# Optimization experiments

Measured on AMD Instinct MI355X. Metric: run time of the kernel, lower is better.

Reference implementation:

```python
import jax, jax.numpy as jnp
import numpy as np


def _gcn_conv(X, src, dst, norm, W, n_nodes):
    # gather + normalized aggregate (SpMM) then dense linear (GEMM)
    msg = X[src] * norm[:, None]                       # [E, F]
    agg = jax.ops.segment_sum(msg, dst, num_segments=n_nodes)  # [N, F]
    return agg @ W                                     # [N, F_out]


def setup_inputs() -> dict:
    key = jax.random.key(0)
    k1, k2, k3, k4, k5 = jax.random.split(key, 5)
    N, E, D_IN, D_HID, D_OUT = 50000, 800000, 128, 128, 64
    X = jax.random.normal(k1, (N, D_IN), dtype=jnp.float32)
    edge_index = jax.random.randint(k2, (2, E), 0, N, dtype=jnp.int64)
    s = 1.0 / np.sqrt(D_IN)
    W1 = jax.random.normal(k3, (D_IN, D_HID), dtype=jnp.float32) * s
    W2 = jax.random.normal(k4, (D_HID, D_HID), dtype=jnp.float32) * s
    W3 = jax.random.normal(k5, (D_HID, D_OUT), dtype=jnp.float32) * s
    return {"X": X, "edge_index": edge_index, "W1": W1, "W2": W2, "W3": W3}


def reference(X, edge_index, W1, W2, W3):
    n_nodes = X.shape[0]
    src, dst = edge_index[0], edge_index[1]
    # symmetric degree normalization D^-1/2 A D^-1/2 (degrees from edge list)
    ones = jnp.ones(src.shape[0], dtype=X.dtype)
    deg = jax.ops.segment_sum(ones, dst, num_segments=n_nodes)
    deg = jnp.maximum(deg, 1.0)
    dinv = jax.lax.rsqrt(deg)
    norm = dinv[src] * dinv[dst]                       # [E]
    h = jax.nn.relu(_gcn_conv(X, src, dst, norm, W1, n_nodes))
    h = jax.nn.relu(_gcn_conv(h, src, dst, norm, W2, n_nodes))
    h = jax.nn.relu(_gcn_conv(h, src, dst, norm, W3, n_nodes))
    return jax.nn.softmax(h, axis=-1)
```

## Files before the change

### kernel.cpp

```cpp
#include <hip/hip_runtime.h>
#include <hip/hip_bf16.h>

typedef __attribute__((ext_vector_type(8))) short short8;
typedef __attribute__((ext_vector_type(4))) short short4v;
typedef __attribute__((ext_vector_type(4))) float f32x4;

static inline size_t ws_align(size_t x) { return (x + 511) & ~((size_t)511); }

static __device__ inline unsigned short f2bf(float f) {
    __hip_bfloat16 h = __float2bfloat16(f);
    return __builtin_bit_cast(unsigned short, h);
}

static __device__ inline float bf2f(unsigned short u) {
    unsigned int x = ((unsigned int)u) << 16;
    return __builtin_bit_cast(float, x);
}

__global__ void sniff_kernel(const unsigned short* __restrict__ w1,
                             const unsigned int* __restrict__ ei,
                             int* __restrict__ flags) {
    int i = threadIdx.x;
    unsigned e = (w1[2 * i] >> 7) & 0xFF;
    unsigned long long m1 = __ballot(e >= 100 && e <= 130);
    unsigned long long m2 = __ballot(ei[2 * i + 1] == 0u);
    if (i == 0) {
        flags[0] = (__popcll(m1) < 48) ? 1 : 0;
        flags[1] = (__popcll(m2) >= 48) ? 1 : 0;
    }
}

__global__ void hist_kernel(const int* __restrict__ ei, const int* __restrict__ flags,
                            int* __restrict__ counts, int* __restrict__ loff, int E) {
    int e = blockIdx.x * blockDim.x + threadIdx.x;
    if (e < E) {
        int d = flags[1] ? ei[2 * (size_t)E + 2 * e] : ei[(size_t)E + e];
        loff[e] = atomicAdd(&counts[d], 1);
    }
}

__global__ __launch_bounds__(256) void alloc_kernel(const int* __restrict__ counts,
                                                    float* __restrict__ dinv,
                                                    int* __restrict__ rowptr,
                                                    int* __restrict__ total, int N) {
    int n = blockIdx.x * blockDim.x + threadIdx.x;
    int lane = threadIdx.x & 63;
    int c = (n < N) ? counts[n] : 0;
    if (n < N) {
        int d = (c < 1) ? 1 : c;
        dinv[n] = rsqrtf((float)d);
    }
    int incl = c;
#pragma unroll
    for (int off = 1; off < 64; off <<= 1) {
        int v = __shfl_up(incl, off, 64);
        if (lane >= off) incl += v;
    }
    int wavetot = __shfl(incl, 63, 64);
    int base = 0;
    if (lane == 0) base = atomicAdd(total, wavetot);
    base = __shfl(base, 0, 64);
    if (n < N) rowptr[n] = base + incl - c;
}

__global__ void fill_kernel(const int* __restrict__ ei, const int* __restrict__ flags,
                            const float* __restrict__ dinv, const int* __restrict__ rowptr,
                            const int* __restrict__ loff, int2* __restrict__ edgedat, int E) {
    int e = blockIdx.x * blockDim.x + threadIdx.x;
    if (e < E) {
        int s, d;
        if (flags[1]) {
            s = ei[2 * e];
            d = ei[2 * (size_t)E + 2 * e];
        } else {
            s = ei[e];
            d = ei[(size_t)E + e];
        }
        int pos = rowptr[d] + loff[e];
        float wt = dinv[s] * dinv[d];
        edgedat[pos] = make_int2(s, __float_as_int(wt));
    }
}


template <int FOUT>
__global__ __launch_bounds__(256) void gemm_kernel(const void* __restrict__ Araw, int a_follows,
                                                   const void* __restrict__ Wraw,
                                                   const int* __restrict__ flags,
                                                   unsigned short* __restrict__ out, int Nrows) {
    constexpr int K = 128;
    constexpr int NT = FOUT / 16;
    constexpr int LDB = K + 8;
    __shared__ __align__(16) unsigned short bt[FOUT * LDB];

    const int tid = threadIdx.x;
    const int in_fp32 = flags[0];
    const int a_fp32 = a_follows & in_fp32;

    constexpr int TOT4 = K * FOUT / 4;
    if (in_fp32) {
        const float* Wf = (const float*)Wraw;
        for (int i = tid; i < TOT4; i += 256) {
            int idx = i * 4;
            int k = idx / FOUT;
            int n = idx & (FOUT - 1);
            float4 v = *(const float4*)(const void*)(Wf + idx);
            bt[(n + 0) * LDB + k] = f2bf(v.x);
            bt[(n + 1) * LDB + k] = f2bf(v.y);
            bt[(n + 2) * LDB + k] = f2bf(v.z);
            bt[(n + 3) * LDB + k] = f2bf(v.w);
        }
    } else {
        const unsigned short* Ws = (const unsigned short*)Wraw;
        for (int i = tid; i < TOT4; i += 256) {
            int idx = i * 4;
            int k = idx / FOUT;
            int n = idx & (FOUT - 1);
            short4v v = *(const short4v*)(const void*)(Ws + idx);
#pragma unroll
            for (int j = 0; j < 4; j++) bt[(n + j) * LDB + k] = ((const unsigned short*)&v)[j];
        }
    }

    const int wave = tid >> 6;
    const int lane = tid & 63;
    const int quad = lane >> 4;
    const int r16 = lane & 15;

    short8 afrag[2][4];
#pragma unroll
    for (int t = 0; t < 2; t++) {
        int arow = blockIdx.x * 128 + t * 64 + wave * 16 + r16;
        if (arow > Nrows - 1) arow = Nrows - 1;
        if (a_fp32) {
            const float* Ap = (const float*)Araw + (size_t)arow * K + quad * 8;
#pragma unroll
            for (int kk = 0; kk < 4; kk++) {
                float4 f0 = *(const float4*)(const void*)(Ap + kk * 32);
                float4 f1 = *(const float4*)(const void*)(Ap + kk * 32 + 4);
                short8 r;
                r[0] = (short)f2bf(f0.x); r[1] = (short)f2bf(f0.y);
                r[2] = (short)f2bf(f0.z); r[3] = (short)f2bf(f0.w);
                r[4] = (short)f2bf(f1.x); r[5] = (short)f2bf(f1.y);
                r[6] = (short)f2bf(f1.z); r[7] = (short)f2bf(f1.w);
                afrag[t][kk] = r;
            }
        } else {
            const unsigned short* Ap = (const unsigned short*)Araw + (size_t)arow * K + quad * 8;
#pragma unroll
            for (int kk = 0; kk < 4; kk++) afrag[t][kk] = *(const short8*)(const void*)(Ap + kk * 32);
        }
    }

    __syncthreads();

    f32x4 acc[2][NT];
#pragma unroll
    for (int t = 0; t < 2; t++)
#pragma unroll
        for (int nt = 0; nt < NT; nt++) acc[t][nt] = (f32x4){0.f, 0.f, 0.f, 0.f};

#pragma unroll
    for (int kk = 0; kk < 4; kk++) {
#pragma unroll
        for (int nt = 0; nt < NT; nt++) {
            short8 b = *(const short8*)(const void*)(&bt[(nt * 16 + r16) * LDB + kk * 32 + quad * 8]);
#pragma unroll
            for (int t = 0; t < 2; t++)
                acc[t][nt] = __builtin_amdgcn_mfma_f32_16x16x32_bf16(afrag[t][kk], b, acc[t][nt], 0, 0, 0);
        }
    }

#pragma unroll
    for (int t = 0; t < 2; t++) {
#pragma unroll
        for (int nt = 0; nt < NT; nt++) {
#pragma unroll
            for (int r = 0; r < 4; r++) {
                float v = acc[t][nt][r];
                float o = __shfl_xor(v, 1, 64);
                int row = blockIdx.x * 128 + t * 64 + wave * 16 + quad * 4 + r;
                if (((lane & 1) == 0) && row < Nrows) {
                    __hip_bfloat162 pk;
                    pk.x = __float2bfloat16(v);
                    pk.y = __float2bfloat16(o);
                    *(__hip_bfloat162*)(out + (size_t)row * FOUT + nt * 16 + r16) = pk;
                }
            }
        }
    }
}


__global__ __launch_bounds__(256) void spmm128_kernel(const int2* __restrict__ edgedat,
                                                      const int* __restrict__ rowptr,
                                                      const int* __restrict__ counts,
                                                      const unsigned short* __restrict__ Hin,
                                                      unsigned short* __restrict__ Hout, int N) {
    int wid = (blockIdx.x * 256 + threadIdx.x) >> 6;
    if (wid >= N) return;
    int lane = threadIdx.x & 63;
    int grp = lane >> 4;
    int gl = lane & 15;
    int n = __builtin_amdgcn_readfirstlane(wid);
    int start = __builtin_amdgcn_readfirstlane(rowptr[n]);
    int len = __builtin_amdgcn_readfirstlane(counts[n]);
    const int2* ep = edgedat + start;

    float acc[8];
#pragma unroll
    for (int u = 0; u < 8; u++) acc[u] = 0.f;

    int j = 0;
    for (; j + 8 <= len; j += 8) {
        int2 e0 = ep[j + grp];
        int2 e1 = ep[j + 4 + grp];
        short8 h0 = *(const short8*)(const void*)(Hin + (size_t)e0.x * 128 + gl * 8);
        short8 h1 = *(const short8*)(const void*)(Hin + (size_t)e1.x * 128 + gl * 8);
        float w0 = __int_as_float(e0.y);
        float w1 = __int_as_float(e1.y);
#pragma unroll
        for (int u = 0; u < 8; u++) acc[u] += w0 * bf2f((unsigned short)h0[u]);
#pragma unroll
        for (int u = 0; u < 8; u++) acc[u] += w1 * bf2f((unsigned short)h1[u]);
    }
    for (; j + 4 <= len; j += 4) {
        int2 e = ep[j + grp];
        short8 h = *(const short8*)(const void*)(Hin + (size_t)e.x * 128 + gl * 8);
        float w = __int_as_float(e.y);
#pragma unroll
        for (int u = 0; u < 8; u++) acc[u] += w * bf2f((unsigned short)h[u]);
    }
    int rem = len - j;
    if (grp < rem) {
        int2 e = ep[j + grp];
        short8 h = *(const short8*)(const void*)(Hin + (size_t)e.x * 128 + gl * 8);
        float w = __int_as_float(e.y);
#pragma unroll
        for (int u = 0; u < 8; u++) acc[u] += w * bf2f((unsigned short)h[u]);
    }

#pragma unroll
    for (int u = 0; u < 8; u++) {
        acc[u] += __shfl_xor(acc[u], 16, 64);
        acc[u] += __shfl_xor(acc[u], 32, 64);
    }

    if (grp == 0) {
        short8 o;
#pragma unroll
        for (int u = 0; u < 8; u++) o[u] = (short)f2bf(fmaxf(acc[u], 0.f));
        *(short8*)(void*)(Hout + (size_t)n * 128 + gl * 8) = o;
    }
}


__global__ __launch_bounds__(256) void spmm64_softmax_kernel(const int2* __restrict__ edgedat,
                                                             const int* __restrict__ rowptr,
                                                             const int* __restrict__ counts,
                                                             const unsigned short* __restrict__ Hin,
                                                             const int* __restrict__ flags,
                                                             void* __restrict__ Out, int N) {
    int wid = (blockIdx.x * 256 + threadIdx.x) >> 6;
    if (wid >= N) return;
    int lane = threadIdx.x & 63;
    int grp = lane >> 3;
    int gl = lane & 7;
    int n = __builtin_amdgcn_readfirstlane(wid);
    int start = __builtin_amdgcn_readfirstlane(rowptr[n]);
    int len = __builtin_amdgcn_readfirstlane(counts[n]);
    const int2* ep = edgedat + start;

    float acc[8];
#pragma unroll
    for (int u = 0; u < 8; u++) acc[u] = 0.f;

    int j = 0;
    for (; j + 16 <= len; j += 16) {
        int2 e0 = ep[j + grp];
        int2 e1 = ep[j + 8 + grp];
        short8 h0 = *(const short8*)(const void*)(Hin + (size_t)e0.x * 64 + gl * 8);
        short8 h1 = *(const short8*)(const void*)(Hin + (size_t)e1.x * 64 + gl * 8);
        float w0 = __int_as_float(e0.y);
        float w1 = __int_as_float(e1.y);
#pragma unroll
        for (int u = 0; u < 8; u++) acc[u] += w0 * bf2f((unsigned short)h0[u]);
#pragma unroll
        for (int u = 0; u < 8; u++) acc[u] += w1 * bf2f((unsigned short)h1[u]);
    }
    for (; j + 8 <= len; j += 8) {
        int2 e = ep[j + grp];
        short8 h = *(const short8*)(const void*)(Hin + (size_t)e.x * 64 + gl * 8);
        float w = __int_as_float(e.y);
#pragma unroll
        for (int u = 0; u < 8; u++) acc[u] += w * bf2f((unsigned short)h[u]);
    }
    int rem = len - j;
    if (grp < rem) {
        int2 e = ep[j + grp];
        short8 h = *(const short8*)(const void*)(Hin + (size_t)e.x * 64 + gl * 8);
        float w = __int_as_float(e.y);
#pragma unroll
        for (int u = 0; u < 8; u++) acc[u] += w * bf2f((unsigned short)h[u]);
    }

#pragma unroll
    for (int u = 0; u < 8; u++) {
        acc[u] += __shfl_xor(acc[u], 8, 64);
        acc[u] += __shfl_xor(acc[u], 16, 64);
        acc[u] += __shfl_xor(acc[u], 32, 64);
    }

#pragma unroll
    for (int u = 0; u < 8; u++) acc[u] = fmaxf(acc[u], 0.f);

    float m = acc[0];
#pragma unroll
    for (int u = 1; u < 8; u++) m = fmaxf(m, acc[u]);
#pragma unroll
    for (int off = 1; off < 8; off <<= 1) m = fmaxf(m, __shfl_xor(m, off, 64));

    float ex[8];
    float s = 0.f;
#pragma unroll
    for (int u = 0; u < 8; u++) {
        ex[u] = __expf(acc[u] - m);
        s += ex[u];
    }
#pragma unroll
    for (int off = 1; off < 8; off <<= 1) s += __shfl_xor(s, off, 64);
    float inv = 1.0f / s;

    if (grp == 0) {
        if (flags[0]) {
            float* op = (float*)Out + (size_t)n * 64 + gl * 8;
            float4 v0, v1;
            v0.x = ex[0] * inv; v0.y = ex[1] * inv; v0.z = ex[2] * inv; v0.w = ex[3] * inv;
            v1.x = ex[4] * inv; v1.y = ex[5] * inv; v1.z = ex[6] * inv; v1.w = ex[7] * inv;
            *(float4*)(void*)op = v0;
            *(float4*)(void*)(op + 4) = v1;
        } else {
            short8 o;
#pragma unroll
            for (int u = 0; u < 8; u++) o[u] = (short)f2bf(ex[u] * inv);
            *(short8*)(void*)((unsigned short*)Out + (size_t)n * 64 + gl * 8) = o;
        }
    }
}


extern "C" void kernel_launch(void* const* d_in, const int* in_sizes, int n_in,
                              void* d_out, int out_size, void* d_ws, size_t ws_size,
                              hipStream_t stream) {
    const void* X  = d_in[0];
    const int*  ei = (const int*)d_in[1];
    const void* W1 = d_in[2];
    const void* W2 = d_in[3];
    const void* W3 = d_in[4];

    const int N = in_sizes[0] / 128;
    const int E = in_sizes[1] / 2;

    char* ws = (char*)d_ws;
    size_t off = 0;
    int* counts = (int*)(ws + off);   off += ws_align((size_t)N * 4);
    int* total  = (int*)(ws + off);   off += ws_align(64);
    const size_t zero_bytes = off;
    int* flags    = (int*)(ws + off);   off += ws_align(64);
    int* rowptr   = (int*)(ws + off);   off += ws_align((size_t)N * 4);
    float* dinv   = (float*)(ws + off); off += ws_align((size_t)N * 4);
    int* loff     = (int*)(ws + off);   off += ws_align((size_t)E * 4);
    int2* edgedat = (int2*)(ws + off);  off += ws_align((size_t)E * 8);
    unsigned short* HA = (unsigned short*)(ws + off); off += ws_align((size_t)N * 128 * 2);
    unsigned short* HB = (unsigned short*)(ws + off); off += ws_align((size_t)N * 128 * 2);

    hipMemsetAsync(d_ws, 0, zero_bytes, stream);

    sniff_kernel<<<1, 64, 0, stream>>>((const unsigned short*)W1, (const unsigned int*)ei, flags);
    hist_kernel<<<(E + 255) / 256, 256, 0, stream>>>(ei, flags, counts, loff, E);
    alloc_kernel<<<(N + 255) / 256, 256, 0, stream>>>(counts, dinv, rowptr, total, N);
    fill_kernel<<<(E + 255) / 256, 256, 0, stream>>>(ei, flags, dinv, rowptr, loff, edgedat, E);

    const int gblocks = (N + 127) / 128;
    const int sblocks = (N * 64 + 255) / 256;

    gemm_kernel<128><<<gblocks, 256, 0, stream>>>(X, 1, W1, flags, HA, N);
    spmm128_kernel<<<sblocks, 256, 0, stream>>>(edgedat, rowptr, counts, HA, HB, N);
    gemm_kernel<128><<<gblocks, 256, 0, stream>>>(HB, 0, W2, flags, HA, N);
    spmm128_kernel<<<sblocks, 256, 0, stream>>>(edgedat, rowptr, counts, HA, HB, N);
    gemm_kernel<64><<<gblocks, 256, 0, stream>>>(HB, 0, W3, flags, HA, N);
    spmm64_softmax_kernel<<<sblocks, 256, 0, stream>>>(edgedat, rowptr, counts, HA, flags, d_out, N);
}
```

Before: 273.9 us.

## Store hidden features in 32-column slices so SpMM gathers stay cache-resident

```diff
diff --git a/kernel.cpp b/kernel.cpp
--- a/kernel.cpp
+++ b/kernel.cpp
@@ -83,7 +83,7 @@
 }
 
 
-template <int FOUT>
+template <int FOUT, bool SLICED_OUT>
 __global__ __launch_bounds__(256) void gemm_kernel(const void* __restrict__ Araw, int a_follows,
                                                    const void* __restrict__ Wraw,
                                                    const int* __restrict__ flags,
@@ -145,10 +145,15 @@
                 r[6] = (short)f2bf(f1.z); r[7] = (short)f2bf(f1.w);
                 afrag[t][kk] = r;
             }
+        } else if (a_follows) {
+            const unsigned short* Ap = (const unsigned short*)Araw + (size_t)arow * K + quad * 8;
+#pragma unroll
+            for (int kk = 0; kk < 4; kk++) afrag[t][kk] = *(const short8*)(const void*)(Ap + kk * 32);
         } else {
-            const unsigned short* Ap = (const unsigned short*)Araw + (size_t)arow * K + quad * 8;
-#pragma unroll
-            for (int kk = 0; kk < 4; kk++) afrag[t][kk] = *(const short8*)(const void*)(Ap + kk * 32);
+            const unsigned short* Ab = (const unsigned short*)Araw;
+#pragma unroll
+            for (int kk = 0; kk < 4; kk++)
+                afrag[t][kk] = *(const short8*)(const void*)(Ab + ((size_t)kk * Nrows + arow) * 32 + quad * 8);
         }
     }
 
@@ -184,7 +189,13 @@
                     __hip_bfloat162 pk;
                     pk.x = __float2bfloat16(v);
                     pk.y = __float2bfloat16(o);
-                    *(__hip_bfloat162*)(out + (size_t)row * FOUT + nt * 16 + r16) = pk;
+                    size_t addr;
+                    if constexpr (SLICED_OUT) {
+                        addr = ((size_t)(nt >> 1) * Nrows + row) * 32 + (nt & 1) * 16 + r16;
+                    } else {
+                        addr = (size_t)row * FOUT + nt * 16 + r16;
+                    }
+                    *(__hip_bfloat162*)(out + addr) = pk;
                 }
             }
         }
@@ -192,41 +203,35 @@
 }
 
 
-__global__ __launch_bounds__(256) void spmm128_kernel(const int2* __restrict__ edgedat,
-                                                      const int* __restrict__ rowptr,
-                                                      const int* __restrict__ counts,
-                                                      const unsigned short* __restrict__ Hin,
-                                                      unsigned short* __restrict__ Hout, int N) {
-    int wid = (blockIdx.x * 256 + threadIdx.x) >> 6;
-    if (wid >= N) return;
+__global__ __launch_bounds__(256) void spmm128s_kernel(const int2* __restrict__ edgedat,
+                                                       const int* __restrict__ rowptr,
+                                                       const int* __restrict__ counts,
+                                                       const unsigned short* __restrict__ Hin,
+                                                       unsigned short* __restrict__ Hout,
+                                                       int N, int nodeblocks) {
+    int bid = blockIdx.x;
+    int slice = bid / nodeblocks;
+    int nb = bid - slice * nodeblocks;
+    int wave = threadIdx.x >> 6;
+    int node = nb * 4 + wave;
+    if (node >= N) return;
     int lane = threadIdx.x & 63;
-    int grp = lane >> 4;
-    int gl = lane & 15;
-    int n = __builtin_amdgcn_readfirstlane(wid);
+    int grp = lane >> 2;
+    int gl = lane & 3;
+    int n = __builtin_amdgcn_readfirstlane(node);
     int start = __builtin_amdgcn_readfirstlane(rowptr[n]);
     int len = __builtin_amdgcn_readfirstlane(counts[n]);
     const int2* ep = edgedat + start;
+    const unsigned short* Hs = Hin + (size_t)slice * N * 32;
 
     float acc[8];
 #pragma unroll
     for (int u = 0; u < 8; u++) acc[u] = 0.f;
 
     int j = 0;
-    for (; j + 8 <= len; j += 8) {
-        int2 e0 = ep[j + grp];
-        int2 e1 = ep[j + 4 + grp];
-        short8 h0 = *(const short8*)(const void*)(Hin + (size_t)e0.x * 128 + gl * 8);
-        short8 h1 = *(const short8*)(const void*)(Hin + (size_t)e1.x * 128 + gl * 8);
-        float w0 = __int_as_float(e0.y);
-        float w1 = __int_as_float(e1.y);
-#pragma unroll
-        for (int u = 0; u < 8; u++) acc[u] += w0 * bf2f((unsigned short)h0[u]);
-#pragma unroll
-        for (int u = 0; u < 8; u++) acc[u] += w1 * bf2f((unsigned short)h1[u]);
-    }
-    for (; j + 4 <= len; j += 4) {
+    for (; j + 16 <= len; j += 16) {
         int2 e = ep[j + grp];
-        short8 h = *(const short8*)(const void*)(Hin + (size_t)e.x * 128 + gl * 8);
+        short8 h = *(const short8*)(const void*)(Hs + (size_t)e.x * 32 + gl * 8);
         float w = __int_as_float(e.y);
 #pragma unroll
         for (int u = 0; u < 8; u++) acc[u] += w * bf2f((unsigned short)h[u]);
@@ -234,7 +239,7 @@
     int rem = len - j;
     if (grp < rem) {
         int2 e = ep[j + grp];
-        short8 h = *(const short8*)(const void*)(Hin + (size_t)e.x * 128 + gl * 8);
+        short8 h = *(const short8*)(const void*)(Hs + (size_t)e.x * 32 + gl * 8);
         float w = __int_as_float(e.y);
 #pragma unroll
         for (int u = 0; u < 8; u++) acc[u] += w * bf2f((unsigned short)h[u]);
@@ -242,6 +247,8 @@
 
 #pragma unroll
     for (int u = 0; u < 8; u++) {
+        acc[u] += __shfl_xor(acc[u], 4, 64);
+        acc[u] += __shfl_xor(acc[u], 8, 64);
         acc[u] += __shfl_xor(acc[u], 16, 64);
         acc[u] += __shfl_xor(acc[u], 32, 64);
     }
@@ -250,7 +257,7 @@
         short8 o;
 #pragma unroll
         for (int u = 0; u < 8; u++) o[u] = (short)f2bf(fmaxf(acc[u], 0.f));
-        *(short8*)(void*)(Hout + (size_t)n * 128 + gl * 8) = o;
+        *(short8*)(void*)(Hout + (size_t)slice * N * 32 + (size_t)n * 32 + gl * 8) = o;
     }
 }
 
@@ -382,12 +389,13 @@
     fill_kernel<<<(E + 255) / 256, 256, 0, stream>>>(ei, flags, dinv, rowptr, loff, edgedat, E);
 
     const int gblocks = (N + 127) / 128;
+    const int nodeblocks = (N + 3) / 4;
     const int sblocks = (N * 64 + 255) / 256;
 
-    gemm_kernel<128><<<gblocks, 256, 0, stream>>>(X, 1, W1, flags, HA, N);
-    spmm128_kernel<<<sblocks, 256, 0, stream>>>(edgedat, rowptr, counts, HA, HB, N);
-    gemm_kernel<128><<<gblocks, 256, 0, stream>>>(HB, 0, W2, flags, HA, N);
-    spmm128_kernel<<<sblocks, 256, 0, stream>>>(edgedat, rowptr, counts, HA, HB, N);
-    gemm_kernel<64><<<gblocks, 256, 0, stream>>>(HB, 0, W3, flags, HA, N);
+    gemm_kernel<128, true><<<gblocks, 256, 0, stream>>>(X, 1, W1, flags, HA, N);
+    spmm128s_kernel<<<4 * nodeblocks, 256, 0, stream>>>(edgedat, rowptr, counts, HA, HB, N, nodeblocks);
+    gemm_kernel<128, true><<<gblocks, 256, 0, stream>>>(HB, 0, W2, flags, HA, N);
+    spmm128s_kernel<<<4 * nodeblocks, 256, 0, stream>>>(edgedat, rowptr, counts, HA, HB, N, nodeblocks);
+    gemm_kernel<64, false><<<gblocks, 256, 0, stream>>>(HB, 0, W3, flags, HA, N);
     spmm64_softmax_kernel<<<sblocks, 256, 0, stream>>>(edgedat, rowptr, counts, HA, flags, d_out, N);
 }
```

Measured after the change: 344.9 us. 1.26x slower.

## Fuse aggregation with GEMM per layer and reorder to aggregate-then-transform

Applied to the files above, without the earlier changes.

```diff
diff --git a/kernel.cpp b/kernel.cpp
--- a/kernel.cpp
+++ b/kernel.cpp
@@ -27,6 +27,31 @@
     if (i == 0) {
         flags[0] = (__popcll(m1) < 48) ? 1 : 0;
         flags[1] = (__popcll(m2) >= 48) ? 1 : 0;
+    }
+}
+
+__global__ __launch_bounds__(256) void xconv_kernel(const void* __restrict__ Xraw,
+                                                    const int* __restrict__ flags,
+                                                    unsigned short* __restrict__ Xb,
+                                                    long long total8) {
+    long long stride = (long long)gridDim.x * 256;
+    if (flags[0]) {
+        const float* Xf = (const float*)Xraw;
+        for (long long i = blockIdx.x * 256LL + threadIdx.x; i < total8; i += stride) {
+            float4 f0 = *(const float4*)(const void*)(Xf + i * 8);
+            float4 f1 = *(const float4*)(const void*)(Xf + i * 8 + 4);
+            short8 r;
+            r[0] = (short)f2bf(f0.x); r[1] = (short)f2bf(f0.y);
+            r[2] = (short)f2bf(f0.z); r[3] = (short)f2bf(f0.w);
+            r[4] = (short)f2bf(f1.x); r[5] = (short)f2bf(f1.y);
+            r[6] = (short)f2bf(f1.z); r[7] = (short)f2bf(f1.w);
+            *(short8*)(void*)(Xb + i * 8) = r;
+        }
+    } else {
+        const unsigned short* Xs = (const unsigned short*)Xraw;
+        for (long long i = blockIdx.x * 256LL + threadIdx.x; i < total8; i += stride) {
+            *(short8*)(void*)(Xb + i * 8) = *(const short8*)(const void*)(Xs + i * 8);
+        }
     }
 }
 
@@ -82,21 +107,11 @@
     }
 }
 
-
 template <int FOUT>
-__global__ __launch_bounds__(256) void gemm_kernel(const void* __restrict__ Araw, int a_follows,
-                                                   const void* __restrict__ Wraw,
-                                                   const int* __restrict__ flags,
-                                                   unsigned short* __restrict__ out, int Nrows) {
+static __device__ inline void stage_w(const void* __restrict__ Wraw, int in_fp32,
+                                      unsigned short* __restrict__ bt, int tid) {
     constexpr int K = 128;
-    constexpr int NT = FOUT / 16;
     constexpr int LDB = K + 8;
-    __shared__ __align__(16) unsigned short bt[FOUT * LDB];
-
-    const int tid = threadIdx.x;
-    const int in_fp32 = flags[0];
-    const int a_fp32 = a_follows & in_fp32;
-
     constexpr int TOT4 = K * FOUT / 4;
     if (in_fp32) {
         const float* Wf = (const float*)Wraw;
@@ -121,139 +136,179 @@
             for (int j = 0; j < 4; j++) bt[(n + j) * LDB + k] = ((const unsigned short*)&v)[j];
         }
     }
+}
+
+
+template <bool FUSE3>
+__global__ __launch_bounds__(256) void fused_layer_kernel(const unsigned short* __restrict__ Hprev,
+                                                          const void* __restrict__ Wraw,
+                                                          const void* __restrict__ W3raw,
+                                                          const int2* __restrict__ edgedat,
+                                                          const int* __restrict__ rowptr,
+                                                          const int* __restrict__ counts,
+                                                          const int* __restrict__ flags,
+                                                          unsigned short* __restrict__ out,
+                                                          int N) {
+    constexpr int LDB = 136;
+    __shared__ __align__(16) unsigned short btW[128 * LDB];
+    __shared__ __align__(16) unsigned short agg[64 * LDB];
+    __shared__ __align__(16) unsigned short btW3[FUSE3 ? 64 * LDB : 8];
+
+    const int tid = threadIdx.x;
+    const int in_fp32 = flags[0];
+
+    stage_w<128>(Wraw, in_fp32, btW, tid);
+    if constexpr (FUSE3) stage_w<64>(W3raw, in_fp32, btW3, tid);
+    __syncthreads();
 
     const int wave = tid >> 6;
     const int lane = tid & 63;
+    const int grp = lane >> 4;
+    const int gl = lane & 15;
+
+    for (int i = 0; i < 16; i++) {
+        int node = blockIdx.x * 64 + wave * 16 + i;
+        int start = 0, len = 0;
+        if (node < N) {
+            start = rowptr[node];
+            len = counts[node];
+        }
+        start = __builtin_amdgcn_readfirstlane(start);
+        len = __builtin_amdgcn_readfirstlane(len);
+        const int2* ep = edgedat + start;
+
+        float acc[8];
+#pragma unroll
+        for (int u = 0; u < 8; u++) acc[u] = 0.f;
+
+        int j = 0;
+        for (; j + 8 <= len; j += 8) {
+            int2 e0 = ep[j + grp];
+            int2 e1 = ep[j + 4 + grp];
+            short8 h0 = *(const short8*)(const void*)(Hprev + (size_t)e0.x * 128 + gl * 8);
+            short8 h1 = *(const short8*)(const void*)(Hprev + (size_t)e1.x * 128 + gl * 8);
+            float w0 = __int_as_float(e0.y);
+            float w1 = __int_as_float(e1.y);
+#pragma unroll
+            for (int u = 0; u < 8; u++) acc[u] += w0 * bf2f((unsigned short)h0[u]);
+#pragma unroll
+            for (int u = 0; u < 8; u++) acc[u] += w1 * bf2f((unsigned short)h1[u]);
+        }
+        for (; j + 4 <= len; j += 4) {
+            int2 e = ep[j + grp];
+            short8 h = *(const short8*)(const void*)(Hprev + (size_t)e.x * 128 + gl * 8);
+            float w = __int_as_float(e.y);
+#pragma unroll
+            for (int u = 0; u < 8; u++) acc[u] += w * bf2f((unsigned short)h[u]);
+        }
+        int rem = len - j;
+        if (grp < rem) {
+            int2 e = ep[j + grp];
+            short8 h = *(const short8*)(const void*)(Hprev + (size_t)e.x * 128 + gl * 8);
+            float w = __int_as_float(e.y);
+#pragma unroll
+            for (int u = 0; u < 8; u++) acc[u] += w * bf2f((unsigned short)h[u]);
+        }
+
+#pragma unroll
+        for (int u = 0; u < 8; u++) {
+            acc[u] += __shfl_xor(acc[u], 16, 64);
+            acc[u] += __shfl_xor(acc[u], 32, 64);
+        }
+
+        if (grp == 0) {
+            short8 o;
+#pragma unroll
+            for (int u = 0; u < 8; u++) o[u] = (short)f2bf(acc[u]);
+            *(short8*)(void*)(&agg[(wave * 16 + i) * LDB + gl * 8]) = o;
+        }
+    }
+
     const int quad = lane >> 4;
     const int r16 = lane & 15;
 
-    short8 afrag[2][4];
-#pragma unroll
-    for (int t = 0; t < 2; t++) {
-        int arow = blockIdx.x * 128 + t * 64 + wave * 16 + r16;
-        if (arow > Nrows - 1) arow = Nrows - 1;
-        if (a_fp32) {
-            const float* Ap = (const float*)Araw + (size_t)arow * K + quad * 8;
-#pragma unroll
-            for (int kk = 0; kk < 4; kk++) {
-                float4 f0 = *(const float4*)(const void*)(Ap + kk * 32);
-                float4 f1 = *(const float4*)(const void*)(Ap + kk * 32 + 4);
-                short8 r;
-                r[0] = (short)f2bf(f0.x); r[1] = (short)f2bf(f0.y);
-                r[2] = (short)f2bf(f0.z); r[3] = (short)f2bf(f0.w);
-                r[4] = (short)f2bf(f1.x); r[5] = (short)f2bf(f1.y);
-                r[6] = (short)f2bf(f1.z); r[7] = (short)f2bf(f1.w);
-                afrag[t][kk] = r;
-            }
-        } else {
-            const unsigned short* Ap = (const unsigned short*)Araw + (size_t)arow * K + quad * 8;
-#pragma unroll
-            for (int kk = 0; kk < 4; kk++) afrag[t][kk] = *(const short8*)(const void*)(Ap + kk * 32);
-        }
-    }
-
-    __syncthreads();
-
-    f32x4 acc[2][NT];
-#pragma unroll
-    for (int t = 0; t < 2; t++)
-#pragma unroll
-        for (int nt = 0; nt < NT; nt++) acc[t][nt] = (f32x4){0.f, 0.f, 0.f, 0.f};
+    short8 afrag[4];
+#pragma unroll
+    for (int kk = 0; kk < 4; kk++)
+        afrag[kk] = *(const short8*)(const void*)(&agg[(wave * 16 + r16) * LDB + kk * 32 + quad * 8]);
+
+    f32x4 acc2[8];
+#pragma unroll
+    for (int nt = 0; nt < 8; nt++) acc2[nt] = (f32x4){0.f, 0.f, 0.f, 0.f};
 
 #pragma unroll
     for (int kk = 0; kk < 4; kk++) {
 #pragma unroll
-        for (int nt = 0; nt < NT; nt++) {
-            short8 b = *(const short8*)(const void*)(&bt[(nt * 16 + r16) * LDB + kk * 32 + quad * 8]);
-#pragma unroll
-            for (int t = 0; t < 2; t++)
-                acc[t][nt] = __builtin_amdgcn_mfma_f32_16x16x32_bf16(afrag[t][kk], b, acc[t][nt], 0, 0, 0);
-        }
-    }
-
-#pragma unroll
-    for (int t = 0; t < 2; t++) {
-#pragma unroll
-        for (int nt = 0; nt < NT; nt++) {
+        for (int nt = 0; nt < 8; nt++) {
+            short8 b = *(const short8*)(const void*)(&btW[(nt * 16 + r16) * LDB + kk * 32 + quad * 8]);
+            acc2[nt] = __builtin_amdgcn_mfma_f32_16x16x32_bf16(afrag[kk], b, acc2[nt], 0, 0, 0);
+        }
+    }
+
+    if constexpr (!FUSE3) {
+#pragma unroll
+        for (int nt = 0; nt < 8; nt++) {
 #pragma unroll
             for (int r = 0; r < 4; r++) {
-                float v = acc[t][nt][r];
+                float v = fmaxf(acc2[nt][r], 0.f);
                 float o = __shfl_xor(v, 1, 64);
-                int row = blockIdx.x * 128 + t * 64 + wave * 16 + quad * 4 + r;
-                if (((lane & 1) == 0) && row < Nrows) {
+                int row = blockIdx.x * 64 + wave * 16 + quad * 4 + r;
+                if (((lane & 1) == 0) && row < N) {
                     __hip_bfloat162 pk;
                     pk.x = __float2bfloat16(v);
                     pk.y = __float2bfloat16(o);
-                    *(__hip_bfloat162*)(out + (size_t)row * FOUT + nt * 16 + r16) = pk;
+                    *(__hip_bfloat162*)(out + (size_t)row * 128 + nt * 16 + r16) = pk;
                 }
             }
         }
-    }
-}
-
-
-__global__ __launch_bounds__(256) void spmm128_kernel(const int2* __restrict__ edgedat,
-                                                      const int* __restrict__ rowptr,
-                                                      const int* __restrict__ counts,
-                                                      const unsigned short* __restrict__ Hin,
-                                                      unsigned short* __restrict__ Hout, int N) {
-    int wid = (blockIdx.x * 256 + threadIdx.x) >> 6;
-    if (wid >= N) return;
-    int lane = threadIdx.x & 63;
-    int grp = lane >> 4;
-    int gl = lane & 15;
-    int n = __builtin_amdgcn_readfirstlane(wid);
-    int start = __builtin_amdgcn_readfirstlane(rowptr[n]);
-    int len = __builtin_amdgcn_readfirstlane(counts[n]);
-    const int2* ep = edgedat + start;
-
-    float acc[8];
-#pragma unroll
-    for (int u = 0; u < 8; u++) acc[u] = 0.f;
-
-    int j = 0;
-    for (; j + 8 <= len; j += 8) {
-        int2 e0 = ep[j + grp];
-        int2 e1 = ep[j + 4 + grp];
-        short8 h0 = *(const short8*)(const void*)(Hin + (size_t)e0.x * 128 + gl * 8);
-        short8 h1 = *(const short8*)(const void*)(Hin + (size_t)e1.x * 128 + gl * 8);
-        float w0 = __int_as_float(e0.y);
-        float w1 = __int_as_float(e1.y);
-#pragma unroll
-        for (int u = 0; u < 8; u++) acc[u] += w0 * bf2f((unsigned short)h0[u]);
-#pragma unroll
-        for (int u = 0; u < 8; u++) acc[u] += w1 * bf2f((unsigned short)h1[u]);
-    }
-    for (; j + 4 <= len; j += 4) {
-        int2 e = ep[j + grp];
-        short8 h = *(const short8*)(const void*)(Hin + (size_t)e.x * 128 + gl * 8);
-        float w = __int_as_float(e.y);
-#pragma unroll
-        for (int u = 0; u < 8; u++) acc[u] += w * bf2f((unsigned short)h[u]);
-    }
-    int rem = len - j;
-    if (grp < rem) {
-        int2 e = ep[j + grp];
-        short8 h = *(const short8*)(const void*)(Hin + (size_t)e.x * 128 + gl * 8);
-        float w = __int_as_float(e.y);
-#pragma unroll
-        for (int u = 0; u < 8; u++) acc[u] += w * bf2f((unsigned short)h[u]);
-    }
-
-#pragma unroll
-    for (int u = 0; u < 8; u++) {
-        acc[u] += __shfl_xor(acc[u], 16, 64);
-        acc[u] += __shfl_xor(acc[u], 32, 64);
-    }
-
-    if (grp == 0) {
-        short8 o;
-#pragma unroll
-        for (int u = 0; u < 8; u++) o[u] = (short)f2bf(fmaxf(acc[u], 0.f));
-        *(short8*)(void*)(Hout + (size_t)n * 128 + gl * 8) = o;
-    }
-}
-
+    } else {
+#pragma unroll
+        for (int nt = 0; nt < 8; nt++) {
+#pragma unroll
+            for (int r = 0; r < 4; r++) {
+                float v = fmaxf(acc2[nt][r], 0.f);
+                float o = __shfl_xor(v, 1, 64);
+                if ((lane & 1) == 0) {
+                    __hip_bfloat162 pk;
+                    pk.x = __float2bfloat16(v);
+                    pk.y = __float2bfloat16(o);
+                    *(__hip_bfloat162*)(&agg[(wave * 16 + quad * 4 + r) * LDB + nt * 16 + r16]) = pk;
+                }
+            }
+        }
+        short8 afrag3[4];
+#pragma unroll
+        for (int kk = 0; kk < 4; kk++)
+            afrag3[kk] = *(const short8*)(const void*)(&agg[(wave * 16 + r16) * LDB + kk * 32 + quad * 8]);
+
+        f32x4 acc3[4];
+#pragma unroll
+        for (int nt = 0; nt < 4; nt++) acc3[nt] = (f32x4){0.f, 0.f, 0.f, 0.f};
+#pragma unroll
+        for (int kk = 0; kk < 4; kk++) {
+#pragma unroll
+            for (int nt = 0; nt < 4; nt++) {
+                short8 b = *(const short8*)(const void*)(&btW3[(nt * 16 + r16) * LDB + kk * 32 + quad * 8]);
+                acc3[nt] = __builtin_amdgcn_mfma_f32_16x16x32_bf16(afrag3[kk], b, acc3[nt], 0, 0, 0);
+            }
+        }
+#pragma unroll
+        for (int nt = 0; nt < 4; nt++) {
+#pragma unroll
+            for (int r = 0; r < 4; r++) {
+                float v = acc3[nt][r];
+                float o = __shfl_xor(v, 1, 64);
+                int row = blockIdx.x * 64 + wave * 16 + quad * 4 + r;
+                if (((lane & 1) == 0) && row < N) {
+                    __hip_bfloat162 pk;
+                    pk.x = __float2bfloat16(v);
+                    pk.y = __float2bfloat16(o);
+                    *(__hip_bfloat162*)(out + (size_t)row * 64 + nt * 16 + r16) = pk;
+                }
+            }
+        }
+    }
+}
 
 __global__ __launch_bounds__(256) void spmm64_softmax_kernel(const int2* __restrict__ edgedat,
                                                              const int* __restrict__ rowptr,
@@ -371,23 +426,29 @@
     float* dinv   = (float*)(ws + off); off += ws_align((size_t)N * 4);
     int* loff     = (int*)(ws + off);   off += ws_align((size_t)E * 4);
     int2* edgedat = (int2*)(ws + off);  off += ws_align((size_t)E * 8);
-    unsigned short* HA = (unsigned short*)(ws + off); off += ws_align((size_t)N * 128 * 2);
-    unsigned short* HB = (unsigned short*)(ws + off); off += ws_align((size_t)N * 128 * 2);
+    unsigned short* Xb = (unsigned short*)(ws + off); off += ws_align((size_t)N * 128 * 2);
+    unsigned short* H1 = (unsigned short*)(ws + off); off += ws_align((size_t)N * 128 * 2);
+    unsigned short* Z3 = (unsigned short*)(ws + off); off += ws_align((size_t)N * 64 * 2);
 
     hipMemsetAsync(d_ws, 0, zero_bytes, stream);
 
     sniff_kernel<<<1, 64, 0, stream>>>((const unsigned short*)W1, (const unsigned int*)ei, flags);
+
+    long long total8 = (long long)N * 16;
+    int cblocks = (int)((total8 + 255) / 256);
+    if (cblocks > 2048) cblocks = 2048;
+    xconv_kernel<<<cblocks, 256, 0, stream>>>(X, flags, Xb, total8);
+
     hist_kernel<<<(E + 255) / 256, 256, 0, stream>>>(ei, flags, counts, loff, E);
     alloc_kernel<<<(N + 255) / 256, 256, 0, stream>>>(counts, dinv, rowptr, total, N);
     fill_kernel<<<(E + 255) / 256, 256, 0, stream>>>(ei, flags, dinv, rowptr, loff, edgedat, E);
 
-    const int gblocks = (N + 127) / 128;
+    const int fblocks = (N + 63) / 64;
     const int sblocks = (N * 64 + 255) / 256;
 
-    gemm_kernel<128><<<gblocks, 256, 0, stream>>>(X, 1, W1, flags, HA, N);
-    spmm128_kernel<<<sblocks, 256, 0, stream>>>(edgedat, rowptr, counts, HA, HB, N);
-    gemm_kernel<128><<<gblocks, 256, 0, stream>>>(HB, 0, W2, flags, HA, N);
-    spmm128_kernel<<<sblocks, 256, 0, stream>>>(edgedat, rowptr, counts, HA, HB, N);
-    gemm_kernel<64><<<gblocks, 256, 0, stream>>>(HB, 0, W3, flags, HA, N);
-    spmm64_softmax_kernel<<<sblocks, 256, 0, stream>>>(edgedat, rowptr, counts, HA, flags, d_out, N);
-}
+    fused_layer_kernel<false><<<fblocks, 256, 0, stream>>>(Xb, W1, nullptr, edgedat, rowptr,
+                                                           counts, flags, H1, N);
+    fused_layer_kernel<true><<<fblocks, 256, 0, stream>>>(H1, W2, W3, edgedat, rowptr,
+                                                          counts, flags, Z3, N);
+    spmm64_softmax_kernel<<<sblocks, 256, 0, stream>>>(edgedat, rowptr, counts, Z3, flags, d_out, N);
+}
```

After: 372.8 us. 36.1% more time.

## Fuse dtype sniffing, degree histogram and first GEMM into one launch

Applied to the files above, without the earlier changes.

```diff
diff --git a/kernel.cpp b/kernel.cpp
--- a/kernel.cpp
+++ b/kernel.cpp
@@ -17,27 +17,135 @@
     return __builtin_bit_cast(float, x);
 }
 
-__global__ void sniff_kernel(const unsigned short* __restrict__ w1,
-                             const unsigned int* __restrict__ ei,
-                             int* __restrict__ flags) {
-    int i = threadIdx.x;
-    unsigned e = (w1[2 * i] >> 7) & 0xFF;
-    unsigned long long m1 = __ballot(e >= 100 && e <= 130);
-    unsigned long long m2 = __ballot(ei[2 * i + 1] == 0u);
-    if (i == 0) {
-        flags[0] = (__popcll(m1) < 48) ? 1 : 0;
-        flags[1] = (__popcll(m2) >= 48) ? 1 : 0;
-    }
-}
-
-__global__ void hist_kernel(const int* __restrict__ ei, const int* __restrict__ flags,
-                            int* __restrict__ counts, int* __restrict__ loff, int E) {
-    int e = blockIdx.x * blockDim.x + threadIdx.x;
-    if (e < E) {
-        int d = flags[1] ? ei[2 * (size_t)E + 2 * e] : ei[(size_t)E + e];
-        loff[e] = atomicAdd(&counts[d], 1);
-    }
-}
+
+__global__ __launch_bounds__(256) void gemm1_hist_kernel(const void* __restrict__ Araw,
+                                                         const unsigned short* __restrict__ w1s,
+                                                         const int* __restrict__ ei,
+                                                         int* __restrict__ counts,
+                                                         int* __restrict__ loff,
+                                                         int* __restrict__ flags,
+                                                         unsigned short* __restrict__ out,
+                                                         int Nrows, int E, int gblocks) {
+    constexpr int K = 128;
+    constexpr int FOUT = 128;
+    constexpr int NT = FOUT / 16;
+    constexpr int LDB = K + 8;
+    __shared__ __align__(16) unsigned short bt[FOUT * LDB];
+
+    const int tid = threadIdx.x;
+    const int lane = tid & 63;
+
+    unsigned ew = (w1s[2 * lane] >> 7) & 0xFF;
+    unsigned long long m1 = __ballot(ew >= 100 && ew <= 130);
+    const int in_fp32 = (__popcll(m1) < 48) ? 1 : 0;
+    unsigned long long m2 = __ballot(((const unsigned int*)ei)[2 * lane + 1] == 0u);
+    const int ei64 = (__popcll(m2) >= 48) ? 1 : 0;
+
+    if (blockIdx.x >= gblocks) {
+        if (blockIdx.x == gblocks && tid == 0) {
+            flags[0] = in_fp32;
+            flags[1] = ei64;
+        }
+        int e = (blockIdx.x - gblocks) * 256 + tid;
+        if (e < E) {
+            int d = ei64 ? ei[2 * (size_t)E + 2 * e] : ei[(size_t)E + e];
+            loff[e] = atomicAdd(&counts[d], 1);
+        }
+        return;
+    }
+
+    constexpr int TOT4 = K * FOUT / 4;
+    if (in_fp32) {
+        const float* Wf = (const float*)(const void*)w1s;
+        for (int i = tid; i < TOT4; i += 256) {
+            int idx = i * 4;
+            int k = idx / FOUT;
+            int n = idx & (FOUT - 1);
+            float4 v = *(const float4*)(const void*)(Wf + idx);
+            bt[(n + 0) * LDB + k] = f2bf(v.x);
+            bt[(n + 1) * LDB + k] = f2bf(v.y);
+            bt[(n + 2) * LDB + k] = f2bf(v.z);
+            bt[(n + 3) * LDB + k] = f2bf(v.w);
+        }
+    } else {
+        for (int i = tid; i < TOT4; i += 256) {
+            int idx = i * 4;
+            int k = idx / FOUT;
+            int n = idx & (FOUT - 1);
+            short4v v = *(const short4v*)(const void*)(w1s + idx);
+#pragma unroll
+            for (int j = 0; j < 4; j++) bt[(n + j) * LDB + k] = ((const unsigned short*)&v)[j];
+        }
+    }
+
+    const int wave = tid >> 6;
+    const int quad = lane >> 4;
+    const int r16 = lane & 15;
+
+    short8 afrag[2][4];
+#pragma unroll
+    for (int t = 0; t < 2; t++) {
+        int arow = blockIdx.x * 128 + t * 64 + wave * 16 + r16;
+        if (arow > Nrows - 1) arow = Nrows - 1;
+        if (in_fp32) {
+            const float* Ap = (const float*)Araw + (size_t)arow * K + quad * 8;
+#pragma unroll
+            for (int kk = 0; kk < 4; kk++) {
+                float4 f0 = *(const float4*)(const void*)(Ap + kk * 32);
+                float4 f1 = *(const float4*)(const void*)(Ap + kk * 32 + 4);
+                short8 r;
+                r[0] = (short)f2bf(f0.x); r[1] = (short)f2bf(f0.y);
+                r[2] = (short)f2bf(f0.z); r[3] = (short)f2bf(f0.w);
+                r[4] = (short)f2bf(f1.x); r[5] = (short)f2bf(f1.y);
+                r[6] = (short)f2bf(f1.z); r[7] = (short)f2bf(f1.w);
+                afrag[t][kk] = r;
+            }
+        } else {
+            const unsigned short* Ap = (const unsigned short*)Araw + (size_t)arow * K + quad * 8;
+#pragma unroll
+            for (int kk = 0; kk < 4; kk++) afrag[t][kk] = *(const short8*)(const void*)(Ap + kk * 32);
+        }
+    }
+
+    __syncthreads();
+
+    f32x4 acc[2][NT];
+#pragma unroll
+    for (int t = 0; t < 2; t++)
+#pragma unroll
+        for (int nt = 0; nt < NT; nt++) acc[t][nt] = (f32x4){0.f, 0.f, 0.f, 0.f};
+
+#pragma unroll
+    for (int kk = 0; kk < 4; kk++) {
+#pragma unroll
+        for (int nt = 0; nt < NT; nt++) {
+            short8 b = *(const short8*)(const void*)(&bt[(nt * 16 + r16) * LDB + kk * 32 + quad * 8]);
+#pragma unroll
+            for (int t = 0; t < 2; t++)
+                acc[t][nt] = __builtin_amdgcn_mfma_f32_16x16x32_bf16(afrag[t][kk], b, acc[t][nt], 0, 0, 0);
+        }
+    }
+
+#pragma unroll
+    for (int t = 0; t < 2; t++) {
+#pragma unroll
+        for (int nt = 0; nt < NT; nt++) {
+#pragma unroll
+            for (int r = 0; r < 4; r++) {
+                float v = acc[t][nt][r];
+                float o = __shfl_xor(v, 1, 64);
+                int row = blockIdx.x * 128 + t * 64 + wave * 16 + quad * 4 + r;
+                if (((lane & 1) == 0) && row < Nrows) {
+                    __hip_bfloat162 pk;
+                    pk.x = __float2bfloat16(v);
+                    pk.y = __float2bfloat16(o);
+                    *(__hip_bfloat162*)(out + (size_t)row * FOUT + nt * 16 + r16) = pk;
+                }
+            }
+        }
+    }
+}
+
 
 __global__ __launch_bounds__(256) void alloc_kernel(const int* __restrict__ counts,
                                                     float* __restrict__ dinv,
@@ -84,7 +192,7 @@
 
 
 template <int FOUT>
-__global__ __launch_bounds__(256) void gemm_kernel(const void* __restrict__ Araw, int a_follows,
+__global__ __launch_bounds__(256) void gemm_kernel(const void* __restrict__ Araw,
                                                    const void* __restrict__ Wraw,
                                                    const int* __restrict__ flags,
                                                    unsigned short* __restrict__ out, int Nrows) {
@@ -95,7 +203,6 @@
 
     const int tid = threadIdx.x;
     const int in_fp32 = flags[0];
-    const int a_fp32 = a_follows & in_fp32;
 
     constexpr int TOT4 = K * FOUT / 4;
     if (in_fp32) {
@@ -132,24 +239,9 @@
     for (int t = 0; t < 2; t++) {
         int arow = blockIdx.x * 128 + t * 64 + wave * 16 + r16;
         if (arow > Nrows - 1) arow = Nrows - 1;
-        if (a_fp32) {
-            const float* Ap = (const float*)Araw + (size_t)arow * K + quad * 8;
-#pragma unroll
-            for (int kk = 0; kk < 4; kk++) {
-                float4 f0 = *(const float4*)(const void*)(Ap + kk * 32);
-                float4 f1 = *(const float4*)(const void*)(Ap + kk * 32 + 4);
-                short8 r;
-                r[0] = (short)f2bf(f0.x); r[1] = (short)f2bf(f0.y);
-                r[2] = (short)f2bf(f0.z); r[3] = (short)f2bf(f0.w);
-                r[4] = (short)f2bf(f1.x); r[5] = (short)f2bf(f1.y);
-                r[6] = (short)f2bf(f1.z); r[7] = (short)f2bf(f1.w);
-                afrag[t][kk] = r;
-            }
-        } else {
-            const unsigned short* Ap = (const unsigned short*)Araw + (size_t)arow * K + quad * 8;
-#pragma unroll
-            for (int kk = 0; kk < 4; kk++) afrag[t][kk] = *(const short8*)(const void*)(Ap + kk * 32);
-        }
+        const unsigned short* Ap = (const unsigned short*)Araw + (size_t)arow * K + quad * 8;
+#pragma unroll
+        for (int kk = 0; kk < 4; kk++) afrag[t][kk] = *(const short8*)(const void*)(Ap + kk * 32);
     }
 
     __syncthreads();
@@ -376,18 +468,18 @@
 
     hipMemsetAsync(d_ws, 0, zero_bytes, stream);
 
-    sniff_kernel<<<1, 64, 0, stream>>>((const unsigned short*)W1, (const unsigned int*)ei, flags);
-    hist_kernel<<<(E + 255) / 256, 256, 0, stream>>>(ei, flags, counts, loff, E);
+    const int gblocks = (N + 127) / 128;
+    const int hblocks = (E + 255) / 256;
+    const int sblocks = (N * 64 + 255) / 256;
+
+    gemm1_hist_kernel<<<gblocks + hblocks, 256, 0, stream>>>(
+        X, (const unsigned short*)W1, ei, counts, loff, flags, HA, N, E, gblocks);
     alloc_kernel<<<(N + 255) / 256, 256, 0, stream>>>(counts, dinv, rowptr, total, N);
-    fill_kernel<<<(E + 255) / 256, 256, 0, stream>>>(ei, flags, dinv, rowptr, loff, edgedat, E);
-
-    const int gblocks = (N + 127) / 128;
-    const int sblocks = (N * 64 + 255) / 256;
-
-    gemm_kernel<128><<<gblocks, 256, 0, stream>>>(X, 1, W1, flags, HA, N);
+    fill_kernel<<<hblocks, 256, 0, stream>>>(ei, flags, dinv, rowptr, loff, edgedat, E);
+
     spmm128_kernel<<<sblocks, 256, 0, stream>>>(edgedat, rowptr, counts, HA, HB, N);
-    gemm_kernel<128><<<gblocks, 256, 0, stream>>>(HB, 0, W2, flags, HA, N);
+    gemm_kernel<128><<<gblocks, 256, 0, stream>>>(HB, W2, flags, HA, N);
     spmm128_kernel<<<sblocks, 256, 0, stream>>>(edgedat, rowptr, counts, HA, HB, N);
-    gemm_kernel<64><<<gblocks, 256, 0, stream>>>(HB, 0, W3, flags, HA, N);
+    gemm_kernel<64><<<gblocks, 256, 0, stream>>>(HB, W3, flags, HA, N);
     spmm64_softmax_kernel<<<sblocks, 256, 0, stream>>>(edgedat, rowptr, counts, HA, flags, d_out, N);
 }
```

Result: faster. 255.0 us (median of 2 runs) (-6.9%).
